# Performance work log

Hardware: AMD Instinct MI355X
Metric: run time of the kernel (lower is better)

## Reference

```python
import jax, jax.numpy as jnp
import numpy as np

# ---- static config (from init_kwargs) ----
B, H, W, C = 4, 256, 256, 96
WS, SS, NH = 8, 4, 3            # window_size, shift_size, num_heads
N = WS * WS                     # tokens per window = 64
NW = (H // WS) * (W // WS)      # windows per image = 1024
HD = C // NH                    # head_dim = 32
SCALE = HD ** -0.5
MLP_H = int(C * 4.0)
EPS = 1e-5


def _relative_position_index():
    coords = np.stack(np.meshgrid(np.arange(WS), np.arange(WS), indexing='ij'))  # (2, WS, WS)
    cf = coords.reshape(2, -1)                       # (2, N)
    rel = (cf[:, :, None] - cf[:, None, :]).transpose(1, 2, 0).astype(np.int64)  # (N, N, 2)
    rel[:, :, 0] += WS - 1
    rel[:, :, 1] += WS - 1
    rel[:, :, 0] *= 2 * WS - 1
    return rel.sum(-1)                               # (N, N) in [0, (2WS-1)^2)


def _attn_mask():
    img = np.zeros((H, W))
    cnt = 0
    slices = (slice(0, -WS), slice(-WS, -SS), slice(-SS, None))
    for hs in slices:
        for ws in slices:
            img[hs, ws] = cnt
            cnt += 1
    m = img.reshape(H // WS, WS, W // WS, WS).transpose(0, 2, 1, 3).reshape(-1, N)  # (NW, N)
    am = m[:, None, :] - m[:, :, None]               # (NW, N, N)
    return np.where(am != 0, -100.0, 0.0).astype(np.float32)


def setup_inputs() -> dict:
    key = jax.random.key(0)
    ks = jax.random.split(key, 8)
    std = 0.02
    inp = {
        'x': jax.random.normal(ks[0], (B, H * W, C), jnp.float32),
        'g1': jnp.ones((C,), jnp.float32),
        'b1': jnp.zeros((C,), jnp.float32),
        'qkv_w': jax.random.normal(ks[1], (3 * C, C), jnp.float32) * std,
        'qkv_b': jnp.zeros((3 * C,), jnp.float32),
        'rpb_table': jax.random.normal(ks[2], ((2 * WS - 1) ** 2, NH), jnp.float32) * std,
        'proj_w': jax.random.normal(ks[3], (C, C), jnp.float32) * std,
        'proj_b': jnp.zeros((C,), jnp.float32),
        'g2': jnp.ones((C,), jnp.float32),
        'b2': jnp.zeros((C,), jnp.float32),
        'fc1_w': jax.random.normal(ks[4], (MLP_H, C), jnp.float32) * std,
        'fc1_b': jnp.zeros((MLP_H,), jnp.float32),
        'fc2_w': jax.random.normal(ks[5], (C, MLP_H), jnp.float32) * std,
        'fc2_b': jnp.zeros((C,), jnp.float32),
        'attn_mask': jnp.asarray(_attn_mask()),
        'rel_index': jnp.asarray(_relative_position_index(), jnp.int32),
    }
    return inp


def _ln(x, g, b):
    mu = jnp.mean(x, -1, keepdims=True)
    var = jnp.mean(jnp.square(x - mu), -1, keepdims=True)
    return (x - mu) * jax.lax.rsqrt(var + EPS) * g + b


def reference(x, g1, b1, qkv_w, qkv_b, rpb_table, proj_w, proj_b,
              g2, b2, fc1_w, fc1_b, fc2_w, fc2_b, attn_mask, rel_index):
    shortcut = x
    h = _ln(x, g1, b1).reshape(B, H, W, C)
    # cyclic shift
    h = jnp.roll(h, (-SS, -SS), axis=(1, 2))
    # window partition -> (B*NW, N, C)
    xw = h.reshape(B, H // WS, WS, W // WS, WS, C).transpose(0, 1, 3, 2, 4, 5).reshape(-1, N, C)
    # qkv projection
    qkv = (xw @ qkv_w.T + qkv_b).reshape(-1, N, 3, NH, HD).transpose(2, 0, 3, 1, 4)  # (3, B_, NH, N, HD)
    q, k, v = qkv[0] * SCALE, qkv[1], qkv[2]
    attn = jnp.einsum('bhnd,bhmd->bhnm', q, k)       # (B_, NH, N, N)
    # gathered relative position bias: (N, N, NH) -> (NH, N, N)
    bias = rpb_table[rel_index].transpose(2, 0, 1)
    attn = attn + bias[None]
    # shifted-window mask
    attn = attn.reshape(B, NW, NH, N, N) + attn_mask[None, :, None]
    attn = jax.nn.softmax(attn.reshape(-1, NH, N, N), axis=-1)
    o = jnp.einsum('bhnm,bhmd->bhnd', attn, v).transpose(0, 2, 1, 3).reshape(-1, N, C)
    o = o @ proj_w.T + proj_b
    # window reverse + reverse shift
    o = o.reshape(B, H // WS, W // WS, WS, WS, C).transpose(0, 1, 3, 2, 4, 5).reshape(B, H, W, C)
    o = jnp.roll(o, (SS, SS), axis=(1, 2)).reshape(B, H * W, C)
    x = shortcut + o
    h2 = _ln(x, g2, b2)
    h2 = jax.nn.gelu(h2 @ fc1_w.T + fc1_b, approximate=False) @ fc2_w.T + fc2_b
    return x + h2
```

## Files before the change

kernel.cpp:

```cpp
#include <hip/hip_runtime.h>
#include <hip/hip_bf16.h>
#include <math.h>

constexpr float SCALE_ = 0.17677669529663687f;

typedef float f32x4 __attribute__((ext_vector_type(4)));
typedef short bf16x8 __attribute__((ext_vector_type(8)));
typedef short short4v __attribute__((ext_vector_type(4)));
#define MFMA __builtin_amdgcn_mfma_f32_16x16x32_bf16


__device__ inline short f2bf(float f) {
    __hip_bfloat16 h = __float2bfloat16(f);
    return *reinterpret_cast<short*>(&h);
}
__device__ inline float bf2f(short s) {
    union { unsigned u; float f; } v; v.u = ((unsigned)(unsigned short)s) << 16;
    return v.f;
}
__device__ inline unsigned pack2bf(float lo, float hi) {
    return (unsigned)(unsigned short)f2bf(lo) |
           ((unsigned)(unsigned short)f2bf(hi) << 16);
}
__device__ inline float gelu_erf(float v) {
    float z  = v * 0.70710678f;
    float z2 = fminf(z * z, 1.5f);
    float p  =      0.00012055333f;
    p = p * z2 -    0.00085483270f;
    p = p * z2 +    0.0052239776f;
    p = p * z2 -    0.0268661706f;
    p = p * z2 +    0.1128379167f;
    p = p * z2 -    0.3761263890f;
    p = p * z2 +    1.1283791671f;
    float er = z * p;
    float t  = 0.5f * v;
    return t * er + t;
}

__global__ __launch_bounds__(256)
void prep_weights(const float* __restrict__ qkv_w, const float* __restrict__ proj_w,
                  const float* __restrict__ fc1_w, const float* __restrict__ fc2_w,
                  short* __restrict__ ws)
{
    int i = blockIdx.x * 256 + threadIdx.x;
    if (i >= 110592) return;
    float v;
    if      (i < 27648)  v = qkv_w[i];
    else if (i < 36864)  v = proj_w[i - 27648];
    else if (i < 73728)  v = fc1_w[i - 36864];
    else                 v = fc2_w[i - 73728];
    ws[i] = f2bf(v);
}

__global__ __launch_bounds__(256)
void prep_comb(const float* __restrict__ rpb, const int* __restrict__ rel,
               const float* __restrict__ mask, short* __restrict__ comb)
{
    int e = blockIdx.x * 256 + threadIdx.x;
    if (e >= 49152) return;
    int t   = e / 12288;
    int rem = e - t * 12288;
    int h   = rem >> 12;
    int ij  = rem & 4095;
    const int rep[4] = {0, 31, 992, 1023};
    comb[e] = f2bf(rpb[rel[ij] * 3 + h] + mask[(long)rep[t] * 4096 + ij]);
}

__global__ __launch_bounds__(256, 3)
void fused_kernel(const float* __restrict__ x,
                  const float* __restrict__ g1, const float* __restrict__ b1,
                  const short* __restrict__ qkv_wb, const float* __restrict__ qkv_b,
                  const short* __restrict__ proj_wb, const float* __restrict__ proj_b,
                  const short* __restrict__ comb,
                  const float* __restrict__ g2, const float* __restrict__ b2,
                  const short* __restrict__ fc1_wb, const float* __restrict__ fc1_b,
                  const short* __restrict__ fc2_wb, const float* __restrict__ fc2_b,
                  float* __restrict__ out)
{
    __shared__ short smem[26880];
    short (*aL)[104]  = (short(*)[104])smem;
    short (*qpL)[104] = (short(*)[104])(smem + 6656);
    short (*kL)[104]  = (short(*)[104])(smem + 13312);
    short (*vT)[72]   = (short(*)[72]) (smem + 19968);
    float (*xmF)[100] = (float(*)[100])(smem + 6656);
    short (*hch)[72]  = (short(*)[72]) (smem + 19456);

    const int tid  = threadIdx.x;
    const int wave = tid >> 6, lane = tid & 63;
    const int lr = lane & 15, lg = lane >> 4;
    const int blk = blockIdx.x;
    const int b = blk >> 10, wi = blk & 1023;
    const int wh = wi >> 5, ww = wi & 31;
    const int mtyp = ((wh == 31) ? 2 : 0) + ((ww == 31) ? 1 : 0);
    const int wm = wave >> 1, wn = wave & 1;

    auto tok_of = [&](int n) -> int {
        int r = n >> 3, c = n & 7;
        int gh = (wh * 8 + r + 4) & 255;
        int gw = (ww * 8 + c + 4) & 255;
        return b * 65536 + gh * 256 + gw;
    };

    {
        const int n = tid >> 2, s = tid & 3;
        const float* xr = x + (long)tok_of(n) * 96 + s * 24;
        float xv[24];
        #pragma unroll
        for (int i = 0; i < 6; i++) {
            float4 t = ((const float4*)xr)[i];
            xv[4*i]=t.x; xv[4*i+1]=t.y; xv[4*i+2]=t.z; xv[4*i+3]=t.w;
        }
        float s1 = 0.f, s2 = 0.f;
        #pragma unroll
        for (int i = 0; i < 24; i++) { s1 += xv[i]; s2 += xv[i]*xv[i]; }
        s1 += __shfl_xor(s1, 1); s2 += __shfl_xor(s2, 1);
        s1 += __shfl_xor(s1, 2); s2 += __shfl_xor(s2, 2);
        float mu = s1 * (1.0f/96.0f);
        float var = s2 * (1.0f/96.0f) - mu*mu;
        float rs = rsqrtf(var + 1e-5f);
        #pragma unroll
        for (int c = 0; c < 12; c++) {
            const int ch = s*24 + 2*c;
            *(unsigned*)&aL[n][ch] =
                pack2bf((xv[2*c  ]-mu)*rs*g1[ch  ] + b1[ch  ],
                        (xv[2*c+1]-mu)*rs*g1[ch+1] + b1[ch+1]);
        }
    }
    __syncthreads();

    {
        bf16x8 afr[2][3];
        #pragma unroll
        for (int mt = 0; mt < 2; mt++)
            #pragma unroll
            for (int kt = 0; kt < 3; kt++)
                afr[mt][kt] = *(const bf16x8*)&aL[(2*wm+mt)*16 + lr][kt*32 + lg*8];
        for (int nt0 = 0; nt0 < 9; nt0++) {
            const int nt = wn * 9 + nt0;
            const int o  = nt * 16 + lr;
            bf16x8 bfr[3];
            #pragma unroll
            for (int kt = 0; kt < 3; kt++)
                bfr[kt] = *(const bf16x8*)&qkv_wb[(long)o * 96 + kt*32 + lg*8];
            const float bias = qkv_b[o];
            #pragma unroll
            for (int mt = 0; mt < 2; mt++) {
                f32x4 acc = {bias, bias, bias, bias};
                #pragma unroll
                for (int kt = 0; kt < 3; kt++)
                    acc = MFMA(afr[mt][kt], bfr[kt], acc, 0, 0, 0);
                const int row0 = (2*wm+mt)*16 + lg*4;
                if (nt < 6) {
                    #pragma unroll
                    for (int r = 0; r < 4; r++) qpL[row0+r][o] = f2bf(acc[r]*SCALE_);
                } else if (nt < 12) {
                    #pragma unroll
                    for (int r = 0; r < 4; r++) kL[row0+r][o-96] = f2bf(acc[r]);
                } else {
                    #pragma unroll
                    for (int r = 0; r < 4; r++) vT[o-192][row0+r] = f2bf(acc[r]);
                }
            }
        }
    }
    __syncthreads();

    bf16x8 qf[3];
    #pragma unroll
    for (int h = 0; h < 3; h++)
        qf[h] = *(const bf16x8*)&qpL[wave*16 + lr][h*32 + lg*8];

    for (int h = 0; h < 3; h++) {
        const short* cb = comb + (mtyp * 3 + h) * 4096;
        float sv[4][4];
        #pragma unroll
        for (int nt = 0; nt < 4; nt++) {
            bf16x8 kf = *(const bf16x8*)&kL[nt*16 + lr][h*32 + lg*8];
            f32x4 s = MFMA(kf, qf[h], (f32x4){0.f,0.f,0.f,0.f}, 0, 0, 0);
            short4v bb = *(const short4v*)&cb[(wave*16 + lr)*64 + nt*16 + lg*4];
            #pragma unroll
            for (int r = 0; r < 4; r++)
                sv[nt][r] = s[r] + bf2f(bb[r]);
        }
        float m = sv[0][0];
        #pragma unroll
        for (int nt = 0; nt < 4; nt++)
            #pragma unroll
            for (int r = 0; r < 4; r++) m = fmaxf(m, sv[nt][r]);
        m = fmaxf(m, __shfl_xor(m, 16));
        m = fmaxf(m, __shfl_xor(m, 32));
        float sum = 0.f;
        #pragma unroll
        for (int nt = 0; nt < 4; nt++)
            #pragma unroll
            for (int r = 0; r < 4; r++) { sv[nt][r] = __expf(sv[nt][r]-m); sum += sv[nt][r]; }
        sum += __shfl_xor(sum, 16);
        sum += __shfl_xor(sum, 32);
        const float inv = 1.0f / sum;
        #pragma unroll
        for (int nt = 0; nt < 4; nt++) {
            uint2 w;
            w.x = pack2bf(sv[nt][0]*inv, sv[nt][1]*inv);
            w.y = pack2bf(sv[nt][2]*inv, sv[nt][3]*inv);
            *(uint2*)&qpL[wave*16 + lr][nt*16 + lg*4] = w;
        }
        bf16x8 pf[2];
        #pragma unroll
        for (int kt = 0; kt < 2; kt++)
            pf[kt] = *(const bf16x8*)&qpL[wave*16 + lr][kt*32 + lg*8];
        #pragma unroll
        for (int nt = 0; nt < 2; nt++) {
            f32x4 acc = {0.f,0.f,0.f,0.f};
            #pragma unroll
            for (int kt = 0; kt < 2; kt++) {
                bf16x8 vf = *(const bf16x8*)&vT[h*32 + nt*16 + lr][kt*32 + lg*8];
                acc = MFMA(vf, pf[kt], acc, 0, 0, 0);
            }
            uint2 w;
            w.x = pack2bf(acc[0], acc[1]);
            w.y = pack2bf(acc[2], acc[3]);
            *(uint2*)&aL[wave*16 + lr][h*32 + nt*16 + lg*4] = w;
        }
    }
    __syncthreads();

    {
        bf16x8 ob[2][3];
        #pragma unroll
        for (int tt = 0; tt < 2; tt++)
            #pragma unroll
            for (int kt = 0; kt < 3; kt++)
                ob[tt][kt] = *(const bf16x8*)&aL[(wn*2+tt)*16 + lr][kt*32 + lg*8];
        #pragma unroll
        for (int ct = 0; ct < 3; ct++) {
            const int cg = wm*3 + ct;
            const int crow = cg*16 + lr;
            bf16x8 pw[3];
            #pragma unroll
            for (int kt = 0; kt < 3; kt++)
                pw[kt] = *(const bf16x8*)&proj_wb[(long)crow * 96 + kt*32 + lg*8];
            const float4 bi = *(const float4*)&proj_b[cg*16 + lg*4];
            #pragma unroll
            for (int tt = 0; tt < 2; tt++) {
                f32x4 acc = {bi.x, bi.y, bi.z, bi.w};
                #pragma unroll
                for (int kt = 0; kt < 3; kt++)
                    acc = MFMA(pw[kt], ob[tt][kt], acc, 0, 0, 0);
                const int tok = (wn*2+tt)*16 + lr;
                const float4 xo = *(const float4*)&x[(long)tok_of(tok) * 96 + cg*16 + lg*4];
                float4 xm;
                xm.x = acc[0] + xo.x; xm.y = acc[1] + xo.y;
                xm.z = acc[2] + xo.z; xm.w = acc[3] + xo.w;
                *(float4*)&xmF[tok][cg*16 + lg*4] = xm;
            }
        }
    }
    __syncthreads();

    {
        const int n = tid >> 2, s = tid & 3;
        float xv[24];
        #pragma unroll
        for (int i = 0; i < 6; i++) {
            float4 t = *(const float4*)&xmF[n][s*24 + 4*i];
            xv[4*i]=t.x; xv[4*i+1]=t.y; xv[4*i+2]=t.z; xv[4*i+3]=t.w;
        }
        float s1 = 0.f, s2 = 0.f;
        #pragma unroll
        for (int i = 0; i < 24; i++) { s1 += xv[i]; s2 += xv[i]*xv[i]; }
        s1 += __shfl_xor(s1, 1); s2 += __shfl_xor(s2, 1);
        s1 += __shfl_xor(s1, 2); s2 += __shfl_xor(s2, 2);
        float mu  = s1 * (1.0f/96.0f);
        float var = s2 * (1.0f/96.0f) - mu*mu;
        float rs  = rsqrtf(var + 1e-5f);
        #pragma unroll
        for (int j = 0; j < 12; j++) {
            const int ch = s*24 + 2*j;
            *(unsigned*)&aL[n][ch] =
                pack2bf((xv[2*j  ]-mu)*rs*g2[ch  ] + b2[ch  ],
                        (xv[2*j+1]-mu)*rs*g2[ch+1] + b2[ch+1]);
        }
    }
    __syncthreads();

    bf16x8 bx[2][3];
    #pragma unroll
    for (int tt = 0; tt < 2; tt++)
        #pragma unroll
        for (int kt = 0; kt < 3; kt++)
            bx[tt][kt] = *(const bf16x8*)&aL[(wn*2+tt)*16 + lr][kt*32 + lg*8];

    f32x4 facc[3][2];
    #pragma unroll
    for (int nt = 0; nt < 3; nt++) {
        const float4 bb = *(const float4*)&fc2_b[(wm*3+nt)*16 + lg*4];
        facc[nt][0] = (f32x4){bb.x, bb.y, bb.z, bb.w};
        facc[nt][1] = facc[nt][0];
    }

    for (int c = 0; c < 6; c++) {
        if (c) __syncthreads();
        #pragma unroll
        for (int h2 = 0; h2 < 2; h2++) {
            const int ht = wm*2 + h2;
            const int o  = c*64 + ht*16 + lr;
            bf16x8 wfr[3];
            #pragma unroll
            for (int kt = 0; kt < 3; kt++)
                wfr[kt] = *(const bf16x8*)&fc1_wb[(long)o * 96 + kt*32 + lg*8];
            const float4 bi = *(const float4*)&fc1_b[c*64 + ht*16 + lg*4];
            #pragma unroll
            for (int tt = 0; tt < 2; tt++) {
                f32x4 acc = {bi.x, bi.y, bi.z, bi.w};
                #pragma unroll
                for (int kt = 0; kt < 3; kt++)
                    acc = MFMA(wfr[kt], bx[tt][kt], acc, 0, 0, 0);
                uint2 w;
                w.x = pack2bf(gelu_erf(acc[0]), gelu_erf(acc[1]));
                w.y = pack2bf(gelu_erf(acc[2]), gelu_erf(acc[3]));
                *(uint2*)&hch[(wn*2+tt)*16 + lr][ht*16 + lg*4] = w;
            }
        }
        __syncthreads();
        #pragma unroll
        for (int tt = 0; tt < 2; tt++) {
            bf16x8 hf[2];
            #pragma unroll
            for (int kt = 0; kt < 2; kt++)
                hf[kt] = *(const bf16x8*)&hch[(wn*2+tt)*16 + lr][kt*32 + lg*8];
            #pragma unroll
            for (int nt = 0; nt < 3; nt++)
                #pragma unroll
                for (int kt = 0; kt < 2; kt++) {
                    bf16x8 wf2 = *(const bf16x8*)&fc2_wb[(long)((wm*3+nt)*16 + lr) * 384 + c*64 + kt*32 + lg*8];
                    facc[nt][tt] = MFMA(wf2, hf[kt], facc[nt][tt], 0, 0, 0);
                }
        }
    }

    #pragma unroll
    for (int nt = 0; nt < 3; nt++)
        #pragma unroll
        for (int tt = 0; tt < 2; tt++) {
            const int tok = (wn*2+tt)*16 + lr;
            const int c0  = (wm*3+nt)*16 + lg*4;
            const float4 xm = *(const float4*)&xmF[tok][c0];
            float4 o;
            o.x = xm.x + facc[nt][tt][0]; o.y = xm.y + facc[nt][tt][1];
            o.z = xm.z + facc[nt][tt][2]; o.w = xm.w + facc[nt][tt][3];
            *(float4*)&out[(long)tok_of(tok) * 96 + c0] = o;
        }
}

extern "C" void kernel_launch(void* const* d_in, const int* in_sizes, int n_in,
                              void* d_out, int out_size, void* d_ws, size_t ws_size,
                              hipStream_t stream)
{
    const float* x      = (const float*)d_in[0];
    const float* g1     = (const float*)d_in[1];
    const float* b1     = (const float*)d_in[2];
    const float* qkv_w  = (const float*)d_in[3];
    const float* qkv_b  = (const float*)d_in[4];
    const float* rpb    = (const float*)d_in[5];
    const float* proj_w = (const float*)d_in[6];
    const float* proj_b = (const float*)d_in[7];
    const float* g2     = (const float*)d_in[8];
    const float* b2     = (const float*)d_in[9];
    const float* fc1_w  = (const float*)d_in[10];
    const float* fc1_b  = (const float*)d_in[11];
    const float* fc2_w  = (const float*)d_in[12];
    const float* fc2_b  = (const float*)d_in[13];
    const float* mask   = (const float*)d_in[14];
    const int*   rel    = (const int*)d_in[15];
    float* out = (float*)d_out;

    short* wsS    = (short*)d_ws;
    short* qkv_wb = wsS;
    short* proj_wb= wsS + 27648;
    short* fc1_wb = wsS + 36864;
    short* fc2_wb = wsS + 73728;
    short* comb   = wsS + 110592;

    prep_weights<<<432, 256, 0, stream>>>(qkv_w, proj_w, fc1_w, fc2_w, wsS);
    prep_comb<<<192, 256, 0, stream>>>(rpb, rel, mask, comb);
    fused_kernel<<<4096, 256, 0, stream>>>(x, g1, b1, qkv_wb, qkv_b,
                                           proj_wb, proj_b, comb,
                                           g2, b2, fc1_wb, fc1_b,
                                           fc2_wb, fc2_b, out);
}
```

Before: 231.3 us.

## Give each wave its own 16 tokens in MLP to drop block barriers

Result: slower. 307.2 us (+32.8%).

```diff
diff --git a/kernel.cpp b/kernel.cpp
--- a/kernel.cpp
+++ b/kernel.cpp
@@ -83,7 +83,7 @@
     short (*kL)[104]  = (short(*)[104])(smem + 13312);
     short (*vT)[72]   = (short(*)[72]) (smem + 19968);
     float (*xmF)[100] = (float(*)[100])(smem + 6656);
-    short (*hch)[72]  = (short(*)[72]) (smem + 19456);
+    short (*hch)[16][72] = (short(*)[16][72])(smem + 19456);
 
     const int tid  = threadIdx.x;
     const int wave = tid >> 6, lane = tid & 63;
@@ -281,75 +281,62 @@
                         (xv[2*j+1]-mu)*rs*g2[ch+1] + b2[ch+1]);
         }
     }
-    __syncthreads();
-
-    bf16x8 bx[2][3];
+
+    bf16x8 bx[3];
     #pragma unroll
-    for (int tt = 0; tt < 2; tt++)
-        #pragma unroll
-        for (int kt = 0; kt < 3; kt++)
-            bx[tt][kt] = *(const bf16x8*)&aL[(wn*2+tt)*16 + lr][kt*32 + lg*8];
-
-    f32x4 facc[3][2];
+    for (int kt = 0; kt < 3; kt++)
+        bx[kt] = *(const bf16x8*)&aL[wave*16 + lr][kt*32 + lg*8];
+
+    f32x4 facc[6];
     #pragma unroll
-    for (int nt = 0; nt < 3; nt++) {
-        const float4 bb = *(const float4*)&fc2_b[(wm*3+nt)*16 + lg*4];
-        facc[nt][0] = (f32x4){bb.x, bb.y, bb.z, bb.w};
-        facc[nt][1] = facc[nt][0];
-    }
-
+    for (int ct = 0; ct < 6; ct++) {
+        const float4 bb = *(const float4*)&fc2_b[ct*16 + lg*4];
+        facc[ct] = (f32x4){bb.x, bb.y, bb.z, bb.w};
+    }
+
+    short (*hw)[72] = hch[wave];
     for (int c = 0; c < 6; c++) {
-        if (c) __syncthreads();
-        #pragma unroll
-        for (int h2 = 0; h2 < 2; h2++) {
-            const int ht = wm*2 + h2;
-            const int o  = c*64 + ht*16 + lr;
+        #pragma unroll
+        for (int ht = 0; ht < 4; ht++) {
+            const int o = c*64 + ht*16 + lr;
             bf16x8 wfr[3];
             #pragma unroll
             for (int kt = 0; kt < 3; kt++)
                 wfr[kt] = *(const bf16x8*)&fc1_wb[(long)o * 96 + kt*32 + lg*8];
             const float4 bi = *(const float4*)&fc1_b[c*64 + ht*16 + lg*4];
-            #pragma unroll
-            for (int tt = 0; tt < 2; tt++) {
-                f32x4 acc = {bi.x, bi.y, bi.z, bi.w};
-                #pragma unroll
-                for (int kt = 0; kt < 3; kt++)
-                    acc = MFMA(wfr[kt], bx[tt][kt], acc, 0, 0, 0);
-                uint2 w;
-                w.x = pack2bf(gelu_erf(acc[0]), gelu_erf(acc[1]));
-                w.y = pack2bf(gelu_erf(acc[2]), gelu_erf(acc[3]));
-                *(uint2*)&hch[(wn*2+tt)*16 + lr][ht*16 + lg*4] = w;
+            f32x4 acc = {bi.x, bi.y, bi.z, bi.w};
+            #pragma unroll
+            for (int kt = 0; kt < 3; kt++)
+                acc = MFMA(wfr[kt], bx[kt], acc, 0, 0, 0);
+            uint2 w;
+            w.x = pack2bf(gelu_erf(acc[0]), gelu_erf(acc[1]));
+            w.y = pack2bf(gelu_erf(acc[2]), gelu_erf(acc[3]));
+            *(uint2*)&hw[lr][ht*16 + lg*4] = w;
+        }
+        bf16x8 hf[2];
+        #pragma unroll
+        for (int kt = 0; kt < 2; kt++)
+            hf[kt] = *(const bf16x8*)&hw[lr][kt*32 + lg*8];
+        #pragma unroll
+        for (int ct = 0; ct < 6; ct++) {
+            #pragma unroll
+            for (int kt = 0; kt < 2; kt++) {
+                bf16x8 wf2 = *(const bf16x8*)&fc2_wb[(long)(ct*16 + lr) * 384 + c*64 + kt*32 + lg*8];
+                facc[ct] = MFMA(wf2, hf[kt], facc[ct], 0, 0, 0);
             }
         }
-        __syncthreads();
-        #pragma unroll
-        for (int tt = 0; tt < 2; tt++) {
-            bf16x8 hf[2];
-            #pragma unroll
-            for (int kt = 0; kt < 2; kt++)
-                hf[kt] = *(const bf16x8*)&hch[(wn*2+tt)*16 + lr][kt*32 + lg*8];
-            #pragma unroll
-            for (int nt = 0; nt < 3; nt++)
-                #pragma unroll
-                for (int kt = 0; kt < 2; kt++) {
-                    bf16x8 wf2 = *(const bf16x8*)&fc2_wb[(long)((wm*3+nt)*16 + lr) * 384 + c*64 + kt*32 + lg*8];
-                    facc[nt][tt] = MFMA(wf2, hf[kt], facc[nt][tt], 0, 0, 0);
-                }
-        }
     }
 
     #pragma unroll
-    for (int nt = 0; nt < 3; nt++)
-        #pragma unroll
-        for (int tt = 0; tt < 2; tt++) {
-            const int tok = (wn*2+tt)*16 + lr;
-            const int c0  = (wm*3+nt)*16 + lg*4;
-            const float4 xm = *(const float4*)&xmF[tok][c0];
-            float4 o;
-            o.x = xm.x + facc[nt][tt][0]; o.y = xm.y + facc[nt][tt][1];
-            o.z = xm.z + facc[nt][tt][2]; o.w = xm.w + facc[nt][tt][3];
-            *(float4*)&out[(long)tok_of(tok) * 96 + c0] = o;
-        }
+    for (int ct = 0; ct < 6; ct++) {
+        const int tok = wave*16 + lr;
+        const int c0  = ct*16 + lg*4;
+        const float4 xm = *(const float4*)&xmF[tok][c0];
+        float4 o;
+        o.x = xm.x + facc[ct][0]; o.y = xm.y + facc[ct][1];
+        o.z = xm.z + facc[ct][2]; o.w = xm.w + facc[ct][3];
+        *(float4*)&out[(long)tok_of(tok) * 96 + c0] = o;
+    }
 }
 
 extern "C" void kernel_launch(void* const* d_in, const int* in_sizes, int n_in,
```
